# Kernel tuning notes

Hardware: AMD Instinct MI355X
Metric: run time of the kernel (lower is better)

## Reference

```python
import jax, jax.numpy as jnp
import numpy as np

N, E, H, D, FE = 50000, 400000, 4, 64, 64  # nodes, edges, heads, per-head dim, edge feat dim
NEG_SLOPE = 0.2


def setup_inputs() -> dict:
    key = jax.random.key(0)
    ks = jax.random.split(key, 18)
    def p(k, shape, s=0.1):
        return jax.random.normal(k, shape, dtype=jnp.float32) * s
    return dict(
        features=p(ks[0], (N, D), 1.0),
        edge_feat=p(ks[1], (E, FE), 1.0),
        src=jax.random.randint(ks[2], (E,), 0, N),
        dst=jax.random.randint(ks[3], (E,), 0, N),
        # layer 0: in=64 -> H*D=256, residual Linear since 64 != 256
        W0=p(ks[4], (D, H * D)), We0=p(ks[5], (FE, H * D)),
        al0=p(ks[6], (H, D)), ar0=p(ks[7], (H, D)), ae0=p(ks[8], (H, D)),
        b0=p(ks[9], (H * D,)), Wres0=p(ks[10], (D, H * D)),
        # layer 1 (last): in=256 -> H*D=256, residual = identity view
        W1=p(ks[11], (H * D, H * D)), We1=p(ks[12], (FE, H * D)),
        al1=p(ks[13], (H, D)), ar1=p(ks[14], (H, D)), ae1=p(ks[15], (H, D)),
        b1=p(ks[16], (H * D,)),
    )


def _edge_gat_layer(h, ef, src, dst, W, We, al, ar, ae, b, Wres=None):
    n = h.shape[0]
    ft = (h @ W).reshape(n, H, D)          # (N,H,D) projected node feats
    fe = (ef @ We).reshape(-1, H, D)       # (E,H,D) projected edge feats
    el = jnp.sum(ft * al, axis=-1)         # (N,H)
    er = jnp.sum(ft * ar, axis=-1)         # (N,H)
    ee = jnp.sum(fe * ae, axis=-1)         # (E,H)
    e = el[src] + er[dst] + ee             # (E,H)
    e = jnp.where(e > 0, e, NEG_SLOPE * e)  # leaky_relu(0.2)
    # segment softmax over incoming edges of each dst node
    m = jax.ops.segment_max(jax.lax.stop_gradient(e), dst, num_segments=n)
    ex = jnp.exp(e - m[dst])
    den = jax.ops.segment_sum(ex, dst, num_segments=n)
    a = ex / den[dst]                      # (E,H) attention
    out = jax.ops.segment_sum(ft[src] * a[:, :, None], dst, num_segments=n)  # (N,H,D)
    res = (h @ Wres).reshape(n, H, D) if Wres is not None else h.reshape(n, H, D)
    return out + res + b.reshape(1, H, D)


def reference(features, edge_feat, src, dst,
              W0, We0, al0, ar0, ae0, b0, Wres0,
              W1, We1, al1, ar1, ae1, b1):
    h = _edge_gat_layer(features, edge_feat, src, dst, W0, We0, al0, ar0, ae0, b0, Wres0)
    h = jax.nn.elu(h.reshape(N, H * D))    # flatten heads + ELU between layers
    h = _edge_gat_layer(h, edge_feat, src, dst, W1, We1, al1, ar1, ae1, b1)
    return h.mean(axis=1)                  # (N, D) mean over heads on last layer
```

## Files before the change

### kernel.cpp

```cpp
#include <hip/hip_runtime.h>
#include <hip/hip_bf16.h>

#define NN 50000
#define EE 400000
#define NB 196

typedef __bf16 bf16_8 __attribute__((ext_vector_type(8)));
typedef __bf16 bf16_2 __attribute__((ext_vector_type(2)));
typedef float f32x4 __attribute__((ext_vector_type(4)));
typedef float f32x2 __attribute__((ext_vector_type(2)));

__device__ inline f32x2 bf2(unsigned u) {
  f32x2 r;
  r.x = __uint_as_float(u << 16);
  r.y = __uint_as_float(u & 0xffff0000u);
  return r;
}

__global__ __launch_bounds__(256) void prep_kernel(
    const float* __restrict__ features, __bf16* __restrict__ fbf,
    const float* __restrict__ W0, const float* __restrict__ Wres0, __bf16* __restrict__ Bt0,
    const float* __restrict__ W1, __bf16* __restrict__ Bt1,
    const float* __restrict__ We0, const float* __restrict__ ae0, float* __restrict__ Ve0,
    const float* __restrict__ We1, const float* __restrict__ ae1, float* __restrict__ Ve1,
    const int* __restrict__ dst, int* __restrict__ cnt) {
  int b = blockIdx.x;
  int t = threadIdx.x;
  if (b < 1563) {
    int i = b * 256 + t;
    if (i < NN * 64 / 8) {
      const float4* p = (const float4*)features + (size_t)i * 2;
      float4 a = p[0], c = p[1];
      bf16_8 v = {(__bf16)a.x, (__bf16)a.y, (__bf16)a.z, (__bf16)a.w,
                  (__bf16)c.x, (__bf16)c.y, (__bf16)c.z, (__bf16)c.w};
      *(bf16_8*)(fbf + (size_t)i * 8) = v;
    }
  } else if (b < 1563 + 128) {
    int idx = (b - 1563) * 256 + t;
    int j = idx >> 6, k = idx & 63;
    float v = (j < 256) ? W0[k * 256 + j] : Wres0[k * 256 + (j - 256)];
    Bt0[idx] = (__bf16)v;
  } else if (b < 1563 + 128 + 256) {
    int idx = (b - 1563 - 128) * 256 + t;
    int j = idx >> 8, k = idx & 255;
    Bt1[idx] = (__bf16)W1[k * 256 + j];
  } else if (b == 1947) {
    int f = t >> 2, h = t & 3;
    float s = 0.f;
    for (int d = 0; d < 64; ++d) s += We0[f * 256 + h * 64 + d] * ae0[h * 64 + d];
    Ve0[f * 4 + h] = s;
  } else if (b == 1948) {
    int f = t >> 2, h = t & 3;
    float s = 0.f;
    for (int d = 0; d < 64; ++d) s += We1[f * 256 + h * 64 + d] * ae1[h * 64 + d];
    Ve1[f * 4 + h] = s;
  } else {
    int e = (b - 1949) * 256 + t;
    if (e < EE) atomicAdd(&cnt[dst[e]], 1);
  }
}

__global__ __launch_bounds__(256) void scan1_kernel(const int* __restrict__ cnt,
                                                    int* __restrict__ scanbuf,
                                                    int* __restrict__ blocksum) {
  __shared__ int s[256];
  int t = threadIdx.x;
  int idx = blockIdx.x * 256 + t;
  int c = (idx < NN) ? cnt[idx] : 0;
  s[t] = c;
  __syncthreads();
  for (int d = 1; d < 256; d <<= 1) {
    int v = (t >= d) ? s[t - d] : 0;
    __syncthreads();
    s[t] += v;
    __syncthreads();
  }
  if (idx < NN) scanbuf[idx] = s[t];
  if (t == 255) blocksum[blockIdx.x] = s[255];
}

__global__ __launch_bounds__(256) void scan23_kernel(const int* __restrict__ scanbuf,
                                                     const int* __restrict__ cnt,
                                                     const int* __restrict__ blocksum,
                                                     int* __restrict__ off,
                                                     int* __restrict__ cur) {
  __shared__ int s[256];
  int t = threadIdx.x;
  int c = (t < NB) ? blocksum[t] : 0;
  s[t] = c;
  __syncthreads();
  for (int d = 1; d < 256; d <<= 1) {
    int v = (t >= d) ? s[t - d] : 0;
    __syncthreads();
    s[t] += v;
    __syncthreads();
  }
  int boff = (blockIdx.x > 0) ? s[blockIdx.x - 1] : 0;
  int idx = blockIdx.x * 256 + t;
  if (idx < NN) {
    int o = boff + scanbuf[idx] - cnt[idx];
    off[idx] = o;
    cur[idx] = o;
  }
  if (idx == 0) off[NN] = EE;
}

__global__ __launch_bounds__(256) void filleek_kernel(
    const int* __restrict__ src, const int* __restrict__ dst,
    int* __restrict__ cur, int* __restrict__ srcc,
    const float* __restrict__ ef, const float* __restrict__ Ve0,
    const float* __restrict__ Ve1, float* __restrict__ eeo0c,
    float* __restrict__ eeo1c) {
  __shared__ float V0[272], V1[272];
  __shared__ int posh[64];
  int t = threadIdx.x;
  int b = blockIdx.x;
  if (t < 64) {
    int e = b * 64 + t;
    int p = atomicAdd(&cur[dst[e]], 1);
    srcc[p] = src[e];
    posh[t] = p;
  }
  V0[t + (t >> 6) * 4] = Ve0[t];
  V1[t + (t >> 6) * 4] = Ve1[t];
  __syncthreads();
  int r = t >> 2, sub = t & 3;
  int e = b * 64 + r;
  float a0 = 0, a1 = 0, a2 = 0, a3 = 0;
  float c0 = 0, c1 = 0, c2 = 0, c3 = 0;
  const float* row = ef + (size_t)e * 64 + sub * 16;
#pragma unroll
  for (int i = 0; i < 16; i += 4) {
    float4 v = *(const float4*)(row + i);
    float xs[4] = {v.x, v.y, v.z, v.w};
#pragma unroll
    for (int j = 0; j < 4; ++j) {
      float x = xs[j];
      int idx = (sub * 16 + i + j) * 4 + sub * 4;
      a0 += x * V0[idx + 0]; a1 += x * V0[idx + 1];
      a2 += x * V0[idx + 2]; a3 += x * V0[idx + 3];
      c0 += x * V1[idx + 0]; c1 += x * V1[idx + 1];
      c2 += x * V1[idx + 2]; c3 += x * V1[idx + 3];
    }
  }
#pragma unroll
  for (int o = 1; o < 4; o <<= 1) {
    a0 += __shfl_xor(a0, o); a1 += __shfl_xor(a1, o);
    a2 += __shfl_xor(a2, o); a3 += __shfl_xor(a3, o);
    c0 += __shfl_xor(c0, o); c1 += __shfl_xor(c1, o);
    c2 += __shfl_xor(c2, o); c3 += __shfl_xor(c3, o);
  }
  if (sub == 0) {
    int p = posh[r];
    float4 u; u.x = a0; u.y = a1; u.z = a2; u.w = a3;
    float4 w; w.x = c0; w.y = c1; w.z = c2; w.w = c3;
    *(float4*)(eeo0c + (size_t)p * 4) = u;
    *(float4*)(eeo1c + (size_t)p * 4) = w;
  }
}

#define LDK 40
__global__ __launch_bounds__(256) void gemm_kernel(const __bf16* __restrict__ A,
                                                   const __bf16* __restrict__ Bt,
                                                   __bf16* __restrict__ ft,
                                                   __bf16* __restrict__ base,
                                                   const float* __restrict__ bias,
                                                   const float* __restrict__ al,
                                                   const float* __restrict__ ar,
                                                   float* __restrict__ el,
                                                   float* __restrict__ er,
                                                   int M, int K) {
  __shared__ __align__(16) __bf16 Al[64 * LDK];
  __shared__ __align__(16) __bf16 Bl[64 * LDK];
  int tid = threadIdx.x;
  int wav = tid >> 6, lane = tid & 63;
  int quad = lane >> 4, l16 = lane & 15;
  int bm = blockIdx.x * 64;
  int bn = blockIdx.y * 64;
  int sr = tid >> 2;
  int sk = (tid & 3) << 3;

  f32x4 acc[4] = {{0, 0, 0, 0}, {0, 0, 0, 0}, {0, 0, 0, 0}, {0, 0, 0, 0}};

  for (int k0 = 0; k0 < K; k0 += 32) {
    uint4 av = {0, 0, 0, 0};
    int arow = bm + sr;
    if (arow < M) av = *(const uint4*)(A + (size_t)arow * K + k0 + sk);
    uint4 bv = *(const uint4*)(Bt + (size_t)(bn + sr) * K + k0 + sk);
    __syncthreads();
    *(uint4*)&Al[sr * LDK + sk] = av;
    *(uint4*)&Bl[sr * LDK + sk] = bv;
    __syncthreads();
    bf16_8 af = *(const bf16_8*)&Al[(wav * 16 + l16) * LDK + quad * 8];
#pragma unroll
    for (int nt = 0; nt < 4; ++nt) {
      bf16_8 bf = *(const bf16_8*)&Bl[(nt * 16 + l16) * LDK + quad * 8];
      acc[nt] = __builtin_amdgcn_mfma_f32_16x16x32_bf16(af, bf, acc[nt], 0, 0, 0);
    }
  }

  int row0 = bm + wav * 16 + quad * 4;

  if (bn < 256) {
    int hb = bn >> 6;
#pragma unroll
    for (int r = 0; r < 4; ++r) {
      float pl = 0.f, pr = 0.f;
#pragma unroll
      for (int nt = 0; nt < 4; ++nt) {
        float v = acc[nt][r];
        int d = nt * 16 + l16;
        pl += v * al[hb * 64 + d];
        pr += v * ar[hb * 64 + d];
      }
#pragma unroll
      for (int o2 = 8; o2 > 0; o2 >>= 1) {
        pl += __shfl_xor(pl, o2);
        pr += __shfl_xor(pr, o2);
      }
      int row = row0 + r;
      if (l16 == 0 && row < M) {
        el[row * 4 + hb] = pl;
        er[row * 4 + hb] = pr;
      }
    }
  }

#pragma unroll
  for (int nt = 0; nt < 4; ++nt) {
    int col = bn + nt * 16 + l16;
#pragma unroll
    for (int r = 0; r < 4; ++r) {
      int row = row0 + r;
      if (row < M) {
        float v = acc[nt][r];
        if (col < 256)
          ft[(size_t)row * 256 + col] = (__bf16)v;
        else
          base[(size_t)row * 256 + (col - 256)] = (__bf16)(v + bias[col - 256]);
      }
    }
  }
}

template <int LAYER>
__global__ __launch_bounds__(256) void agg_kernel(const int* __restrict__ off,
                                                  const int* __restrict__ srcc,
                                                  const float* __restrict__ eeoc,
                                                  const float* __restrict__ el,
                                                  const float* __restrict__ er,
                                                  const __bf16* __restrict__ ft,
                                                  const __bf16* prev,
                                                  const float* __restrict__ bias,
                                                  __bf16* outb,
                                                  float* __restrict__ outf) {
  __shared__ f32x2 wl2[2][4][32];
  __shared__ f32x2 red2[2][4][32];
  int t = threadIdx.x;
  int wav = t >> 6, lane = t & 63;
  int nh = wav >> 1;
  int hf = lane >> 5;
  int head = ((wav & 1) << 1) + hf;
  int k32 = lane & 31;
  int n = blockIdx.x * 2 + nh;
  int beg = off[n], end = off[n + 1];
  float ern = er[n * 4 + head];
  int offb = head * 128 + k32 * 4;

  const char* ftb = (const char*)ft;
  f32x2 acc0 = {0.f, 0.f}, acc1 = {0.f, 0.f};
  float denp = 0.f;

  for (int c = beg; c < end; c += 32) {
    int rem = end - c;
    if (rem > 32) rem = 32;
    int sv = 0;
    float wv = 0.f;
    if (k32 < rem) {
      sv = srcc[c + k32];
      float z = el[sv * 4 + head] + ern + eeoc[(size_t)(c + k32) * 4 + head];
      wv = __expf(z > 0.f ? z : 0.2f * z);
    }
    denp += wv;
    f32x2 wd = {wv, wv};
    wl2[nh][head][k32] = wd;
    int kk = 0;
    for (; kk + 8 <= rem; kk += 8) {
      int s0 = __builtin_amdgcn_readlane(sv, kk);
      int s1 = __builtin_amdgcn_readlane(sv, kk + 1);
      int s2 = __builtin_amdgcn_readlane(sv, kk + 2);
      int s3 = __builtin_amdgcn_readlane(sv, kk + 3);
      int s4 = __builtin_amdgcn_readlane(sv, kk + 4);
      int s5 = __builtin_amdgcn_readlane(sv, kk + 5);
      int s6 = __builtin_amdgcn_readlane(sv, kk + 6);
      int s7 = __builtin_amdgcn_readlane(sv, kk + 7);
      unsigned u0 = *(const unsigned*)(ftb + (size_t)s0 * 512 + offb);
      unsigned u1 = *(const unsigned*)(ftb + (size_t)s1 * 512 + offb);
      unsigned u2 = *(const unsigned*)(ftb + (size_t)s2 * 512 + offb);
      unsigned u3 = *(const unsigned*)(ftb + (size_t)s3 * 512 + offb);
      unsigned u4 = *(const unsigned*)(ftb + (size_t)s4 * 512 + offb);
      unsigned u5 = *(const unsigned*)(ftb + (size_t)s5 * 512 + offb);
      unsigned u6 = *(const unsigned*)(ftb + (size_t)s6 * 512 + offb);
      unsigned u7 = *(const unsigned*)(ftb + (size_t)s7 * 512 + offb);
      f32x2 w0 = wl2[nh][head][kk];
      f32x2 w1 = wl2[nh][head][kk + 1];
      f32x2 w2 = wl2[nh][head][kk + 2];
      f32x2 w3 = wl2[nh][head][kk + 3];
      f32x2 w4 = wl2[nh][head][kk + 4];
      f32x2 w5 = wl2[nh][head][kk + 5];
      f32x2 w6 = wl2[nh][head][kk + 6];
      f32x2 w7 = wl2[nh][head][kk + 7];
      acc0 = __builtin_elementwise_fma(bf2(u0), w0, acc0);
      acc1 = __builtin_elementwise_fma(bf2(u1), w1, acc1);
      acc0 = __builtin_elementwise_fma(bf2(u2), w2, acc0);
      acc1 = __builtin_elementwise_fma(bf2(u3), w3, acc1);
      acc0 = __builtin_elementwise_fma(bf2(u4), w4, acc0);
      acc1 = __builtin_elementwise_fma(bf2(u5), w5, acc1);
      acc0 = __builtin_elementwise_fma(bf2(u6), w6, acc0);
      acc1 = __builtin_elementwise_fma(bf2(u7), w7, acc1);
    }
    for (; kk + 4 <= rem; kk += 4) {
      int s0 = __builtin_amdgcn_readlane(sv, kk);
      int s1 = __builtin_amdgcn_readlane(sv, kk + 1);
      int s2 = __builtin_amdgcn_readlane(sv, kk + 2);
      int s3 = __builtin_amdgcn_readlane(sv, kk + 3);
      unsigned u0 = *(const unsigned*)(ftb + (size_t)s0 * 512 + offb);
      unsigned u1 = *(const unsigned*)(ftb + (size_t)s1 * 512 + offb);
      unsigned u2 = *(const unsigned*)(ftb + (size_t)s2 * 512 + offb);
      unsigned u3 = *(const unsigned*)(ftb + (size_t)s3 * 512 + offb);
      f32x2 w0 = wl2[nh][head][kk];
      f32x2 w1 = wl2[nh][head][kk + 1];
      f32x2 w2 = wl2[nh][head][kk + 2];
      f32x2 w3 = wl2[nh][head][kk + 3];
      acc0 = __builtin_elementwise_fma(bf2(u0), w0, acc0);
      acc1 = __builtin_elementwise_fma(bf2(u1), w1, acc1);
      acc0 = __builtin_elementwise_fma(bf2(u2), w2, acc0);
      acc1 = __builtin_elementwise_fma(bf2(u3), w3, acc1);
    }
    for (; kk < rem; ++kk) {
      int s0 = __builtin_amdgcn_readlane(sv, kk);
      unsigned u0 = *(const unsigned*)(ftb + (size_t)s0 * 512 + offb);
      f32x2 w0 = wl2[nh][head][kk];
      acc0 = __builtin_elementwise_fma(bf2(u0), w0, acc0);
    }
  }
#pragma unroll
  for (int m = 16; m; m >>= 1) denp += __shfl_xor(denp, m);

  f32x2 res = {0.f, 0.f};
  if (end > beg) {
    float rd = 1.f / denp;
    res.x = (acc0.x + acc1.x) * rd;
    res.y = (acc0.y + acc1.y) * rd;
  }

  unsigned pu = *(const unsigned*)((const char*)prev + (size_t)n * 512 + offb);
  f32x2 pv = bf2(pu);

  if (LAYER == 0) {
    float vx = res.x + pv.x;
    float vy = res.y + pv.y;
    vx = vx > 0.f ? vx : (__expf(vx) - 1.0f);
    vy = vy > 0.f ? vy : (__expf(vy) - 1.0f);
    bf16_2 o = {(__bf16)vx, (__bf16)vy};
    *(bf16_2*)((char*)outb + (size_t)n * 512 + offb) = o;
  } else {
    f32x2 bv = *(const f32x2*)(bias + head * 64 + 2 * k32);
    f32x2 rv = {res.x + pv.x + bv.x, res.y + pv.y + bv.y};
    red2[nh][head][k32] = rv;
    __syncthreads();
    if ((wav & 1) == 0 && hf == 0) {
      f32x2 a = red2[nh][0][k32];
      f32x2 b = red2[nh][1][k32];
      f32x2 c = red2[nh][2][k32];
      f32x2 d = red2[nh][3][k32];
      f32x2 s = {0.25f * (a.x + b.x + c.x + d.x), 0.25f * (a.y + b.y + c.y + d.y)};
      *(f32x2*)(outf + (size_t)n * 64 + 2 * k32) = s;
    }
  }
}

extern "C" void kernel_launch(void* const* d_in, const int* in_sizes, int n_in,
                              void* d_out, int out_size, void* d_ws, size_t ws_size,
                              hipStream_t stream) {
  const float* features  = (const float*)d_in[0];
  const float* edge_feat = (const float*)d_in[1];
  const int*   src       = (const int*)d_in[2];
  const int*   dst       = (const int*)d_in[3];
  const float* W0    = (const float*)d_in[4];
  const float* We0   = (const float*)d_in[5];
  const float* al0   = (const float*)d_in[6];
  const float* ar0   = (const float*)d_in[7];
  const float* ae0   = (const float*)d_in[8];
  const float* b0    = (const float*)d_in[9];
  const float* Wres0 = (const float*)d_in[10];
  const float* W1    = (const float*)d_in[11];
  const float* We1   = (const float*)d_in[12];
  const float* al1   = (const float*)d_in[13];
  const float* ar1   = (const float*)d_in[14];
  const float* ae1   = (const float*)d_in[15];
  const float* b1    = (const float*)d_in[16];
  float* out = (float*)d_out;

  char* ws = (char*)d_ws;
  size_t o = 0;
  auto alloc = [&](size_t bytes) {
    void* p = ws + o;
    o = (o + bytes + 255) & ~(size_t)255;
    return p;
  };
  int*    cnt      = (int*)alloc((size_t)NN * 4);
  int*    scanbuf  = (int*)alloc((size_t)NN * 4);
  int*    blocksum = (int*)alloc(256 * 4);
  int*    off      = (int*)alloc((size_t)(NN + 1) * 4);
  int*    cur      = (int*)alloc((size_t)NN * 4);
  int*    srcc     = (int*)alloc((size_t)EE * 4);
  float*  eeo0c    = (float*)alloc((size_t)EE * 4 * 4);
  float*  eeo1c    = (float*)alloc((size_t)EE * 4 * 4);
  float*  el       = (float*)alloc((size_t)NN * 4 * 4);
  float*  er       = (float*)alloc((size_t)NN * 4 * 4);
  float*  Ve0      = (float*)alloc(256 * 4);
  float*  Ve1      = (float*)alloc(256 * 4);
  __bf16* Bt0      = (__bf16*)alloc((size_t)512 * 64 * 2);
  __bf16* Bt1      = (__bf16*)alloc((size_t)256 * 256 * 2);
  __bf16* fbf      = (__bf16*)alloc((size_t)NN * 64 * 2);
  __bf16* ft       = (__bf16*)alloc((size_t)NN * 256 * 2);
  __bf16* base     = (__bf16*)alloc((size_t)NN * 256 * 2);
  __bf16* h1       = base;

  const int EB = (EE + 255) / 256;
  const int MG = (NN + 63) / 64;

  hipMemsetAsync(cnt, 0, (size_t)NN * 4, stream);
  prep_kernel<<<1949 + EB, 256, 0, stream>>>(features, fbf, W0, Wres0, Bt0, W1, Bt1,
                                             We0, ae0, Ve0, We1, ae1, Ve1, dst, cnt);
  scan1_kernel<<<NB, 256, 0, stream>>>(cnt, scanbuf, blocksum);
  scan23_kernel<<<NB, 256, 0, stream>>>(scanbuf, cnt, blocksum, off, cur);
  filleek_kernel<<<EE / 64, 256, 0, stream>>>(src, dst, cur, srcc, edge_feat,
                                              Ve0, Ve1, eeo0c, eeo1c);

  gemm_kernel<<<dim3(MG, 8), 256, 0, stream>>>(fbf, Bt0, ft, base, b0, al0, ar0, el, er, NN, 64);
  agg_kernel<0><<<NN / 2, 256, 0, stream>>>(off, srcc, eeo0c, el, er, ft, base, nullptr, h1, nullptr);

  gemm_kernel<<<dim3(MG, 4), 256, 0, stream>>>(h1, Bt1, ft, nullptr, nullptr, al1, ar1, el, er, NN, 256);
  agg_kernel<1><<<NN / 2, 256, 0, stream>>>(off, srcc, eeo1c, el, er, ft, h1, b1, nullptr, out);
}
```

Before: 387.6 us.

## Map one wavefront per destination node with 8-byte gathers in aggregation

The aggregation kernel now assigns a whole 64-lane wavefront to each destination node. Each lane loads 4 bf16 values (8 bytes) of the 256-wide row, and edges are processed in chunks of 16, with 16 lanes per head computing the attention weights. The layer-1 head mean now uses cross-lane shuffles instead of a shared-memory reduction and __syncthreads. This halves the number of gather instructions per edge and removes the block barrier. In exchange, only 16 edges per chunk get their weights computed in parallel, and the shared weight array is padded.

```diff
diff --git a/kernel.cpp b/kernel.cpp
--- a/kernel.cpp
+++ b/kernel.cpp
@@ -6,6 +6,7 @@
 #define NB 196
 
 typedef __bf16 bf16_8 __attribute__((ext_vector_type(8)));
+typedef __bf16 bf16_4 __attribute__((ext_vector_type(4)));
 typedef __bf16 bf16_2 __attribute__((ext_vector_type(2)));
 typedef float f32x4 __attribute__((ext_vector_type(4)));
 typedef float f32x2 __attribute__((ext_vector_type(2)));
@@ -254,36 +255,32 @@
                                                   const float* __restrict__ bias,
                                                   __bf16* outb,
                                                   float* __restrict__ outf) {
-  __shared__ f32x2 wl2[2][4][32];
-  __shared__ f32x2 red2[2][4][32];
+  __shared__ f32x2 wl2[4][16][5];
   int t = threadIdx.x;
   int wav = t >> 6, lane = t & 63;
-  int nh = wav >> 1;
-  int hf = lane >> 5;
-  int head = ((wav & 1) << 1) + hf;
-  int k32 = lane & 31;
-  int n = blockIdx.x * 2 + nh;
+  int es = lane & 15;
+  int head = lane >> 4;
+  int n = blockIdx.x * 4 + wav;
   int beg = off[n], end = off[n + 1];
   float ern = er[n * 4 + head];
-  int offb = head * 128 + k32 * 4;
+  int offb = lane * 8;
 
   const char* ftb = (const char*)ft;
   f32x2 acc0 = {0.f, 0.f}, acc1 = {0.f, 0.f};
   float denp = 0.f;
 
-  for (int c = beg; c < end; c += 32) {
+  for (int c = beg; c < end; c += 16) {
     int rem = end - c;
-    if (rem > 32) rem = 32;
+    if (rem > 16) rem = 16;
     int sv = 0;
     float wv = 0.f;
-    if (k32 < rem) {
-      sv = srcc[c + k32];
-      float z = el[sv * 4 + head] + ern + eeoc[(size_t)(c + k32) * 4 + head];
+    if (es < rem) {
+      sv = srcc[c + es];
+      float z = el[sv * 4 + head] + ern + eeoc[(size_t)(c + es) * 4 + head];
       wv = __expf(z > 0.f ? z : 0.2f * z);
     }
     denp += wv;
-    f32x2 wd = {wv, wv};
-    wl2[nh][head][k32] = wd;
+    wl2[wav][es][head] = (f32x2){wv, wv};
     int kk = 0;
     for (; kk + 8 <= rem; kk += 8) {
       int s0 = __builtin_amdgcn_readlane(sv, kk);
@@ -294,88 +291,105 @@
       int s5 = __builtin_amdgcn_readlane(sv, kk + 5);
       int s6 = __builtin_amdgcn_readlane(sv, kk + 6);
       int s7 = __builtin_amdgcn_readlane(sv, kk + 7);
-      unsigned u0 = *(const unsigned*)(ftb + (size_t)s0 * 512 + offb);
-      unsigned u1 = *(const unsigned*)(ftb + (size_t)s1 * 512 + offb);
-      unsigned u2 = *(const unsigned*)(ftb + (size_t)s2 * 512 + offb);
-      unsigned u3 = *(const unsigned*)(ftb + (size_t)s3 * 512 + offb);
-      unsigned u4 = *(const unsigned*)(ftb + (size_t)s4 * 512 + offb);
-      unsigned u5 = *(const unsigned*)(ftb + (size_t)s5 * 512 + offb);
-      unsigned u6 = *(const unsigned*)(ftb + (size_t)s6 * 512 + offb);
-      unsigned u7 = *(const unsigned*)(ftb + (size_t)s7 * 512 + offb);
-      f32x2 w0 = wl2[nh][head][kk];
-      f32x2 w1 = wl2[nh][head][kk + 1];
-      f32x2 w2 = wl2[nh][head][kk + 2];
-      f32x2 w3 = wl2[nh][head][kk + 3];
-      f32x2 w4 = wl2[nh][head][kk + 4];
-      f32x2 w5 = wl2[nh][head][kk + 5];
-      f32x2 w6 = wl2[nh][head][kk + 6];
-      f32x2 w7 = wl2[nh][head][kk + 7];
-      acc0 = __builtin_elementwise_fma(bf2(u0), w0, acc0);
-      acc1 = __builtin_elementwise_fma(bf2(u1), w1, acc1);
-      acc0 = __builtin_elementwise_fma(bf2(u2), w2, acc0);
-      acc1 = __builtin_elementwise_fma(bf2(u3), w3, acc1);
-      acc0 = __builtin_elementwise_fma(bf2(u4), w4, acc0);
-      acc1 = __builtin_elementwise_fma(bf2(u5), w5, acc1);
-      acc0 = __builtin_elementwise_fma(bf2(u6), w6, acc0);
-      acc1 = __builtin_elementwise_fma(bf2(u7), w7, acc1);
+      uint2 u0 = *(const uint2*)(ftb + (size_t)s0 * 512 + offb);
+      uint2 u1 = *(const uint2*)(ftb + (size_t)s1 * 512 + offb);
+      uint2 u2 = *(const uint2*)(ftb + (size_t)s2 * 512 + offb);
+      uint2 u3 = *(const uint2*)(ftb + (size_t)s3 * 512 + offb);
+      uint2 u4 = *(const uint2*)(ftb + (size_t)s4 * 512 + offb);
+      uint2 u5 = *(const uint2*)(ftb + (size_t)s5 * 512 + offb);
+      uint2 u6 = *(const uint2*)(ftb + (size_t)s6 * 512 + offb);
+      uint2 u7 = *(const uint2*)(ftb + (size_t)s7 * 512 + offb);
+      f32x2 w0 = wl2[wav][kk][head];
+      f32x2 w1 = wl2[wav][kk + 1][head];
+      f32x2 w2 = wl2[wav][kk + 2][head];
+      f32x2 w3 = wl2[wav][kk + 3][head];
+      f32x2 w4 = wl2[wav][kk + 4][head];
+      f32x2 w5 = wl2[wav][kk + 5][head];
+      f32x2 w6 = wl2[wav][kk + 6][head];
+      f32x2 w7 = wl2[wav][kk + 7][head];
+      acc0 = __builtin_elementwise_fma(bf2(u0.x), w0, acc0);
+      acc1 = __builtin_elementwise_fma(bf2(u0.y), w0, acc1);
+      acc0 = __builtin_elementwise_fma(bf2(u1.x), w1, acc0);
+      acc1 = __builtin_elementwise_fma(bf2(u1.y), w1, acc1);
+      acc0 = __builtin_elementwise_fma(bf2(u2.x), w2, acc0);
+      acc1 = __builtin_elementwise_fma(bf2(u2.y), w2, acc1);
+      acc0 = __builtin_elementwise_fma(bf2(u3.x), w3, acc0);
+      acc1 = __builtin_elementwise_fma(bf2(u3.y), w3, acc1);
+      acc0 = __builtin_elementwise_fma(bf2(u4.x), w4, acc0);
+      acc1 = __builtin_elementwise_fma(bf2(u4.y), w4, acc1);
+      acc0 = __builtin_elementwise_fma(bf2(u5.x), w5, acc0);
+      acc1 = __builtin_elementwise_fma(bf2(u5.y), w5, acc1);
+      acc0 = __builtin_elementwise_fma(bf2(u6.x), w6, acc0);
+      acc1 = __builtin_elementwise_fma(bf2(u6.y), w6, acc1);
+      acc0 = __builtin_elementwise_fma(bf2(u7.x), w7, acc0);
+      acc1 = __builtin_elementwise_fma(bf2(u7.y), w7, acc1);
     }
     for (; kk + 4 <= rem; kk += 4) {
       int s0 = __builtin_amdgcn_readlane(sv, kk);
       int s1 = __builtin_amdgcn_readlane(sv, kk + 1);
       int s2 = __builtin_amdgcn_readlane(sv, kk + 2);
       int s3 = __builtin_amdgcn_readlane(sv, kk + 3);
-      unsigned u0 = *(const unsigned*)(ftb + (size_t)s0 * 512 + offb);
-      unsigned u1 = *(const unsigned*)(ftb + (size_t)s1 * 512 + offb);
-      unsigned u2 = *(const unsigned*)(ftb + (size_t)s2 * 512 + offb);
-      unsigned u3 = *(const unsigned*)(ftb + (size_t)s3 * 512 + offb);
-      f32x2 w0 = wl2[nh][head][kk];
-      f32x2 w1 = wl2[nh][head][kk + 1];
-      f32x2 w2 = wl2[nh][head][kk + 2];
-      f32x2 w3 = wl2[nh][head][kk + 3];
-      acc0 = __builtin_elementwise_fma(bf2(u0), w0, acc0);
-      acc1 = __builtin_elementwise_fma(bf2(u1), w1, acc1);
-      acc0 = __builtin_elementwise_fma(bf2(u2), w2, acc0);
-      acc1 = __builtin_elementwise_fma(bf2(u3), w3, acc1);
+      uint2 u0 = *(const uint2*)(ftb + (size_t)s0 * 512 + offb);
+      uint2 u1 = *(const uint2*)(ftb + (size_t)s1 * 512 + offb);
+      uint2 u2 = *(const uint2*)(ftb + (size_t)s2 * 512 + offb);
+      uint2 u3 = *(const uint2*)(ftb + (size_t)s3 * 512 + offb);
+      f32x2 w0 = wl2[wav][kk][head];
+      f32x2 w1 = wl2[wav][kk + 1][head];
+      f32x2 w2 = wl2[wav][kk + 2][head];
+      f32x2 w3 = wl2[wav][kk + 3][head];
+      acc0 = __builtin_elementwise_fma(bf2(u0.x), w0, acc0);
+      acc1 = __builtin_elementwise_fma(bf2(u0.y), w0, acc1);
+      acc0 = __builtin_elementwise_fma(bf2(u1.x), w1, acc0);
+      acc1 = __builtin_elementwise_fma(bf2(u1.y), w1, acc1);
+      acc0 = __builtin_elementwise_fma(bf2(u2.x), w2, acc0);
+      acc1 = __builtin_elementwise_fma(bf2(u2.y), w2, acc1);
+      acc0 = __builtin_elementwise_fma(bf2(u3.x), w3, acc0);
+      acc1 = __builtin_elementwise_fma(bf2(u3.y), w3, acc1);
     }
     for (; kk < rem; ++kk) {
       int s0 = __builtin_amdgcn_readlane(sv, kk);
-      unsigned u0 = *(const unsigned*)(ftb + (size_t)s0 * 512 + offb);
-      f32x2 w0 = wl2[nh][head][kk];
-      acc0 = __builtin_elementwise_fma(bf2(u0), w0, acc0);
-    }
-  }
-#pragma unroll
-  for (int m = 16; m; m >>= 1) denp += __shfl_xor(denp, m);
-
-  f32x2 res = {0.f, 0.f};
+      uint2 u0 = *(const uint2*)(ftb + (size_t)s0 * 512 + offb);
+      f32x2 w0 = wl2[wav][kk][head];
+      acc0 = __builtin_elementwise_fma(bf2(u0.x), w0, acc0);
+      acc1 = __builtin_elementwise_fma(bf2(u0.y), w0, acc1);
+    }
+  }
+#pragma unroll
+  for (int m = 1; m < 16; m <<= 1) denp += __shfl_xor(denp, m);
+
+  float r0 = 0.f, r1 = 0.f, r2 = 0.f, r3 = 0.f;
   if (end > beg) {
     float rd = 1.f / denp;
-    res.x = (acc0.x + acc1.x) * rd;
-    res.y = (acc0.y + acc1.y) * rd;
-  }
-
-  unsigned pu = *(const unsigned*)((const char*)prev + (size_t)n * 512 + offb);
-  f32x2 pv = bf2(pu);
+    r0 = acc0.x * rd; r1 = acc0.y * rd;
+    r2 = acc1.x * rd; r3 = acc1.y * rd;
+  }
+
+  uint2 pu = *(const uint2*)((const char*)prev + (size_t)n * 512 + offb);
+  f32x2 p0 = bf2(pu.x), p1 = bf2(pu.y);
 
   if (LAYER == 0) {
-    float vx = res.x + pv.x;
-    float vy = res.y + pv.y;
-    vx = vx > 0.f ? vx : (__expf(vx) - 1.0f);
-    vy = vy > 0.f ? vy : (__expf(vy) - 1.0f);
-    bf16_2 o = {(__bf16)vx, (__bf16)vy};
-    *(bf16_2*)((char*)outb + (size_t)n * 512 + offb) = o;
+    float v0 = r0 + p0.x, v1 = r1 + p0.y;
+    float v2 = r2 + p1.x, v3 = r3 + p1.y;
+    v0 = v0 > 0.f ? v0 : (__expf(v0) - 1.0f);
+    v1 = v1 > 0.f ? v1 : (__expf(v1) - 1.0f);
+    v2 = v2 > 0.f ? v2 : (__expf(v2) - 1.0f);
+    v3 = v3 > 0.f ? v3 : (__expf(v3) - 1.0f);
+    bf16_4 o = {(__bf16)v0, (__bf16)v1, (__bf16)v2, (__bf16)v3};
+    *(bf16_4*)((char*)outb + (size_t)n * 512 + offb) = o;
   } else {
-    f32x2 bv = *(const f32x2*)(bias + head * 64 + 2 * k32);
-    f32x2 rv = {res.x + pv.x + bv.x, res.y + pv.y + bv.y};
-    red2[nh][head][k32] = rv;
-    __syncthreads();
-    if ((wav & 1) == 0 && hf == 0) {
-      f32x2 a = red2[nh][0][k32];
-      f32x2 b = red2[nh][1][k32];
-      f32x2 c = red2[nh][2][k32];
-      f32x2 d = red2[nh][3][k32];
-      f32x2 s = {0.25f * (a.x + b.x + c.x + d.x), 0.25f * (a.y + b.y + c.y + d.y)};
-      *(f32x2*)(outf + (size_t)n * 64 + 2 * k32) = s;
+    float4 bv = *(const float4*)(bias + lane * 4);
+    float s0 = r0 + p0.x + bv.x;
+    float s1 = r1 + p0.y + bv.y;
+    float s2 = r2 + p1.x + bv.z;
+    float s3 = r3 + p1.y + bv.w;
+    s0 += __shfl_xor(s0, 16); s0 += __shfl_xor(s0, 32);
+    s1 += __shfl_xor(s1, 16); s1 += __shfl_xor(s1, 32);
+    s2 += __shfl_xor(s2, 16); s2 += __shfl_xor(s2, 32);
+    s3 += __shfl_xor(s3, 16); s3 += __shfl_xor(s3, 32);
+    if (head == 0) {
+      float4 s;
+      s.x = 0.25f * s0; s.y = 0.25f * s1; s.z = 0.25f * s2; s.w = 0.25f * s3;
+      *(float4*)(outf + (size_t)n * 64 + es * 4) = s;
     }
   }
 }
@@ -440,8 +454,8 @@
                                               Ve0, Ve1, eeo0c, eeo1c);
 
   gemm_kernel<<<dim3(MG, 8), 256, 0, stream>>>(fbf, Bt0, ft, base, b0, al0, ar0, el, er, NN, 64);
-  agg_kernel<0><<<NN / 2, 256, 0, stream>>>(off, srcc, eeo0c, el, er, ft, base, nullptr, h1, nullptr);
+  agg_kernel<0><<<NN / 4, 256, 0, stream>>>(off, srcc, eeo0c, el, er, ft, base, nullptr, h1, nullptr);
 
   gemm_kernel<<<dim3(MG, 4), 256, 0, stream>>>(h1, Bt1, ft, nullptr, nullptr, al1, ar1, el, er, NN, 256);
-  agg_kernel<1><<<NN / 2, 256, 0, stream>>>(off, srcc, eeo1c, el, er, ft, h1, b1, nullptr, out);
-}
+  agg_kernel<1><<<NN / 4, 256, 0, stream>>>(off, srcc, eeo1c, el, er, ft, h1, b1, nullptr, out);
+}
```

New measurement: 368.4 us. 5.0% less time.
